# Kernel optimization log

Measured on AMD Instinct MI355X. Metric: run time of the kernel, lower is better.

Reference implementation:

```python
import jax, jax.numpy as jnp
import numpy as np

N, E, H, IN_NF, G, STEPS, EHID = 4096, 8192, 128, 64, 8, 3, 32


def setup_inputs() -> dict:
    key = jax.random.key(0)
    ks = jax.random.split(key, 24)

    def gn(k, shape, fan_in):
        return jax.random.normal(k, shape, dtype=jnp.float32) / np.sqrt(fan_in)

    inp = {
        "x": jax.random.normal(ks[0], (N, IN_NF), dtype=jnp.float32),
        "edge_index": jax.random.randint(ks[1], (2, E), 0, N, dtype=jnp.int32),
        "edge_attr": jax.random.uniform(ks[2], (E, 1), dtype=jnp.float32),
        "batch": jnp.sort(jax.random.randint(ks[3], (N,), 0, G, dtype=jnp.int32)),
        # lin0: in_nf -> hid
        "lin0_w": gn(ks[4], (IN_NF, H), IN_NF),
        "lin0_b": jnp.zeros((H,), jnp.float32),
        # per-step edge MLP: 1 -> 32 -> H*H (stacked over STEPS)
        "nn_w1": gn(ks[5], (STEPS, 1, EHID), 1),
        "nn_b1": jnp.zeros((STEPS, EHID), jnp.float32),
        "nn_w2": gn(ks[6], (STEPS, EHID, H * H), EHID) * 0.1,
        "nn_b2": jnp.zeros((STEPS, H * H), jnp.float32),
        # NNConv root weight (no bias) + conv bias, per step
        "root_w": gn(ks[7], (STEPS, H, H), H),
        "conv_b": jnp.zeros((STEPS, H), jnp.float32),
        # single-layer GRU (input H, hidden H); gate order r, z, n
        "gru_wih": gn(ks[8], (3 * H, H), H),
        "gru_whh": gn(ks[9], (3 * H, H), H),
        "gru_bih": jnp.zeros((3 * H,), jnp.float32),
        "gru_bhh": jnp.zeros((3 * H,), jnp.float32),
        # readout
        "lin1_w": gn(ks[10], (H, H // 2), H),
        "lin1_b": jnp.zeros((H // 2,), jnp.float32),
        "lin2_w": gn(ks[11], (H // 2, 1), H // 2),
        "lin2_b": jnp.zeros((1,), jnp.float32),
    }
    return inp


def _gru_cell(m, h, wih, whh, bih, bhh):
    gi = m @ wih.T + bih          # [N, 3H]
    gh = h @ whh.T + bhh          # [N, 3H]
    i_r, i_z, i_n = jnp.split(gi, 3, axis=-1)
    h_r, h_z, h_n = jnp.split(gh, 3, axis=-1)
    r = jax.nn.sigmoid(i_r + h_r)
    z = jax.nn.sigmoid(i_z + h_z)
    n = jnp.tanh(i_n + r * h_n)
    return (1.0 - z) * n + z * h


def reference(x, edge_index, edge_attr, batch, lin0_w, lin0_b, nn_w1, nn_b1,
              nn_w2, nn_b2, root_w, conv_b, gru_wih, gru_whh, gru_bih,
              gru_bhh, lin1_w, lin1_b, lin2_w, lin2_b):
    n_nodes = x.shape[0]
    row, col = edge_index[0], edge_index[1]  # source j -> target i

    x = jax.nn.relu(x @ lin0_w + lin0_b)     # [N, H]
    h = x

    # in-degree for mean aggregation (0-degree nodes -> 0 output)
    deg = jax.ops.segment_sum(jnp.ones((row.shape[0],), x.dtype), col,
                              num_segments=n_nodes)
    inv_deg = jnp.where(deg > 0, 1.0 / jnp.maximum(deg, 1.0), 0.0)[:, None]

    for t in range(STEPS):
        # edge-conditioned weights: [E, H, H]
        e_h = jax.nn.relu(edge_attr @ nn_w1[t] + nn_b1[t])
        w_e = (e_h @ nn_w2[t] + nn_b2[t]).reshape(-1, H, H)
        # gather -> per-edge matvec -> scatter-mean
        msg = jnp.einsum('eh,eho->eo', x[row], w_e)
        agg = jax.ops.segment_sum(msg, col, num_segments=n_nodes) * inv_deg
        m = jax.nn.relu(agg + x @ root_w[t] + conv_b[t])
        h = _gru_cell(m, h, gru_wih, gru_whh, gru_bih, gru_bhh)
        x = h

    # global mean pool over graphs
    cnt = jax.ops.segment_sum(jnp.ones((n_nodes,), x.dtype), batch,
                              num_segments=G)
    g = jax.ops.segment_sum(x, batch, num_segments=G) / jnp.maximum(cnt, 1.0)[:, None]
    g = jax.nn.relu(g @ lin1_w + lin1_b)  # dropout: eval mode (identity)
    out = g @ lin2_w + lin2_b             # [G, 1]
    return out
```

## Files before the change

kernel.cpp:

```cpp
#include <hip/hip_runtime.h>
#include <math.h>

#define NN 4096
#define EE 8192
#define HH 128
#define GG 8
#define ULD 4352

typedef __attribute__((ext_vector_type(8))) _Float16 half8;
typedef __attribute__((ext_vector_type(4))) float floatx4;

__device__ __forceinline__ void ldst16(const _Float16* g, void* l) {
    __builtin_amdgcn_global_load_lds(
        (const __attribute__((address_space(1))) unsigned int*)g,
        (__attribute__((address_space(3))) unsigned int*)l, 16, 0, 0);
}

__global__ __launch_bounds__(256) void mgemm16_k(
    const _Float16* __restrict__ A, const _Float16* __restrict__ B,
    _Float16* __restrict__ C, const int* __restrict__ kflag)
{
    const int kk = blockIdx.x;
    int cbase;
    if (kk < 32) {
        const unsigned f = *(const unsigned*)kflag;
        if (!((f >> kk) & 1u)) return;
        cbase = __popc(f & ((1u << kk) - 1u)) << 7;
    } else {
        cbase = kk << 7;
    }

    __shared__ __align__(16) _Float16 As[128 * 32];
    __shared__ __align__(16) _Float16 Bs[128 * 32];
    const int tid = threadIdx.x;
    const int lane = tid & 63, wave = tid >> 6;
    const int m0 = blockIdx.y * 128, n0 = kk * 128;
    const int wr = (wave >> 1) * 64, wc = (wave & 1) * 64;
    const int fm = lane & 15, fq = lane >> 4;

    const int srow = tid >> 2, soff = (tid & 3) << 3;
    const _Float16* gA0 = A + (size_t)(m0 + srow) * 128 + soff;
    const _Float16* gA1 = gA0 + (size_t)64 * 128;
    const _Float16* gB0 = B + (size_t)(n0 + srow) * 128 + soff;
    const _Float16* gB1 = gB0 + (size_t)64 * 128;
    char* lA0 = (char*)As + tid * 16;  char* lA1 = (char*)As + (tid + 256) * 16;
    char* lB0 = (char*)Bs + tid * 16;  char* lB1 = (char*)Bs + (tid + 256) * 16;

    floatx4 acc[4][4] = {};
    for (int k0 = 0; k0 < 128; k0 += 32) {
        __syncthreads();
        ldst16(gA0 + k0, lA0); ldst16(gA1 + k0, lA1);
        ldst16(gB0 + k0, lB0); ldst16(gB1 + k0, lB1);
        __syncthreads();
        half8 af[4], bf[4];
#pragma unroll
        for (int i = 0; i < 4; ++i)
            af[i] = *(const half8*)&As[(wr + i * 16 + fm) * 32 + fq * 8];
#pragma unroll
        for (int j = 0; j < 4; ++j)
            bf[j] = *(const half8*)&Bs[(wc + j * 16 + fm) * 32 + fq * 8];
#pragma unroll
        for (int i = 0; i < 4; ++i)
#pragma unroll
            for (int j = 0; j < 4; ++j)
                acc[i][j] = __builtin_amdgcn_mfma_f32_16x16x32_f16(
                    af[i], bf[j], acc[i][j], 0, 0, 0);
    }
    const int er = fq * 4, ec = fm;
#pragma unroll
    for (int i = 0; i < 4; ++i) {
        const int gr = m0 + wr + i * 16 + er;
#pragma unroll
        for (int j = 0; j < 4; ++j) {
            const int gc = cbase + wc + j * 16 + ec;
#pragma unroll
            for (int r = 0; r < 4; ++r)
                C[(size_t)(gr + r) * ULD + gc] = (_Float16)acc[i][j][r];
        }
    }
}

__global__ __launch_bounds__(256) void gru_k(
    const _Float16* __restrict__ bigC, const float* __restrict__ agg,
    const float* __restrict__ cb, const _Float16* __restrict__ Ax,
    const _Float16* __restrict__ Bih, const _Float16* __restrict__ Bhh,
    const float* __restrict__ bih, const float* __restrict__ bhh,
    float* __restrict__ g1, float* __restrict__ g2)
{
    const int z = blockIdx.z;
    const _Float16* B = z ? Bhh : Bih;
    const float* bias = z ? bhh : bih;
    float* C = z ? g2 : g1;

    __shared__ __align__(16) _Float16 As[128 * 40];
    __shared__ __align__(16) _Float16 Bs[128 * 40];
    const int tid = threadIdx.x;
    const int lane = tid & 63, wave = tid >> 6;
    const int m0 = blockIdx.y * 128, n0 = blockIdx.x * 128;
    const int wr = (wave >> 1) * 64, wc = (wave & 1) * 64;
    const int fm = lane & 15, fq = lane >> 4;

    floatx4 acc[4][4] = {};
    for (int k0 = 0; k0 < 128; k0 += 32) {
        __syncthreads();
#pragma unroll
        for (int c = tid; c < 512; c += 256) {
            const int row = c >> 2, seg = (c & 3) << 3;
            if (z == 0) {
                const int mr = m0 + row;
                const half8 cv = *(const half8*)&bigC[(size_t)mr * ULD + 4224 + k0 + seg];
                const float4 a0 = *(const float4*)&agg[(size_t)mr * 128 + k0 + seg];
                const float4 a1 = *(const float4*)&agg[(size_t)mr * 128 + k0 + seg + 4];
                const float4 c0 = *(const float4*)&cb[k0 + seg];
                const float4 c1 = *(const float4*)&cb[k0 + seg + 4];
                _Float16 v8[8];
                float v;
                v = (float)cv[0] + a0.x + c0.x; v8[0] = (_Float16)(v > 0.f ? v : 0.f);
                v = (float)cv[1] + a0.y + c0.y; v8[1] = (_Float16)(v > 0.f ? v : 0.f);
                v = (float)cv[2] + a0.z + c0.z; v8[2] = (_Float16)(v > 0.f ? v : 0.f);
                v = (float)cv[3] + a0.w + c0.w; v8[3] = (_Float16)(v > 0.f ? v : 0.f);
                v = (float)cv[4] + a1.x + c1.x; v8[4] = (_Float16)(v > 0.f ? v : 0.f);
                v = (float)cv[5] + a1.y + c1.y; v8[5] = (_Float16)(v > 0.f ? v : 0.f);
                v = (float)cv[6] + a1.z + c1.z; v8[6] = (_Float16)(v > 0.f ? v : 0.f);
                v = (float)cv[7] + a1.w + c1.w; v8[7] = (_Float16)(v > 0.f ? v : 0.f);
                *(half8*)&As[row * 40 + seg] = *(half8*)v8;
            } else {
                *(half8*)&As[row * 40 + seg] =
                    *(const half8*)&Ax[(size_t)(m0 + row) * 128 + k0 + seg];
            }
            *(half8*)&Bs[row * 40 + seg] =
                *(const half8*)&B[(size_t)(n0 + row) * 128 + k0 + seg];
        }
        __syncthreads();
        half8 af[4], bf[4];
#pragma unroll
        for (int i = 0; i < 4; ++i)
            af[i] = *(const half8*)&As[(wr + i * 16 + fm) * 40 + fq * 8];
#pragma unroll
        for (int j = 0; j < 4; ++j)
            bf[j] = *(const half8*)&Bs[(wc + j * 16 + fm) * 40 + fq * 8];
#pragma unroll
        for (int i = 0; i < 4; ++i)
#pragma unroll
            for (int j = 0; j < 4; ++j)
                acc[i][j] = __builtin_amdgcn_mfma_f32_16x16x32_f16(
                    af[i], bf[j], acc[i][j], 0, 0, 0);
    }
    const int er = fq * 4, ec = fm;
#pragma unroll
    for (int i = 0; i < 4; ++i) {
        const int gr = m0 + wr + i * 16 + er;
#pragma unroll
        for (int j = 0; j < 4; ++j) {
            const int gc = n0 + wc + j * 16 + ec;
            const float bv = bias[gc];
#pragma unroll
            for (int r = 0; r < 4; ++r)
                C[(size_t)(gr + r) * 384 + gc] = acc[i][j][r] + bv;
        }
    }
}

__global__ void gate_k(const float* __restrict__ G1, const float* __restrict__ G2,
                       float* __restrict__ xh, _Float16* __restrict__ Ax,
                       const int* __restrict__ batch, float* __restrict__ pooled) {
    const int idx = blockIdx.x * 256 + threadIdx.x;
    const int n = idx >> 7, o = idx & 127;
    const size_t b = (size_t)n * 384;
    float ir = G1[b + o], iz = G1[b + 128 + o], in_ = G1[b + 256 + o];
    float hr = G2[b + o], hz = G2[b + 128 + o], hn = G2[b + 256 + o];
    float r = 1.f / (1.f + expf(-(ir + hr)));
    float z = 1.f / (1.f + expf(-(iz + hz)));
    float nv = tanhf(in_ + r * hn);
    float hv = (1.f - z) * nv + z * xh[idx];
    xh[idx] = hv;
    Ax[idx] = (_Float16)hv;
    if (pooled) atomicAdd(&pooled[batch[n] * 128 + o], hv);
}

__global__ __launch_bounds__(256) void setup_lin0_k(
    const float* __restrict__ wih, const float* __restrict__ whh,
    _Float16* __restrict__ Bih, _Float16* __restrict__ Bhh,
    const int* __restrict__ ei, const int* __restrict__ batch,
    float* __restrict__ deg, int* __restrict__ odeg, float* __restrict__ cnt,
    const float* __restrict__ x, const float* __restrict__ l0w,
    const float* __restrict__ l0b, float* __restrict__ xh,
    _Float16* __restrict__ Ax)
{
    __shared__ float loc8[GG];
    __shared__ float As[16][64];
    __shared__ float Bs[16][64];
    const int b = blockIdx.x, t = threadIdx.x;
    if (b < 192) {
        const int idx = b * 256 + t;
        Bih[idx] = (_Float16)wih[idx];
        Bhh[idx] = (_Float16)whh[idx];
    } else if (b < 224) {
        const int e = (b - 192) * 256 + t;
        atomicAdd(&deg[ei[EE + e]], 1.0f);
        atomicAdd(&odeg[ei[e]], 1);
    } else if (b < 240) {
        const int n = (b - 224) * 256 + t;
        if (t < GG) loc8[t] = 0.f;
        __syncthreads();
        atomicAdd(&loc8[batch[n]], 1.0f);
        __syncthreads();
        if (t < GG) atomicAdd(&cnt[t], loc8[t]);
    } else {
        const int bb = b - 240;
        const int j0 = (bb & 1) * 64;
        const int m0 = (bb >> 1) * 64;
        const int tx = t & 15, ty = t >> 4;
        const int arow = t >> 2, acol = (t & 3) << 2;
        const int bk = t >> 4, bj = (t & 15) << 2;
        float c[4][4] = {};
        for (int k0 = 0; k0 < 64; k0 += 16) {
            __syncthreads();
            float4 av = *(const float4*)&x[(size_t)(m0 + arow) * 64 + k0 + acol];
            As[acol + 0][arow] = av.x;
            As[acol + 1][arow] = av.y;
            As[acol + 2][arow] = av.z;
            As[acol + 3][arow] = av.w;
            *(float4*)&Bs[bk][bj] = *(const float4*)&l0w[(size_t)(k0 + bk) * 128 + j0 + bj];
            __syncthreads();
#pragma unroll
            for (int kk = 0; kk < 16; ++kk) {
                const float4 a = *(const float4*)&As[kk][ty << 2];
                const float4 bv = *(const float4*)&Bs[kk][tx << 2];
                c[0][0] += a.x * bv.x; c[0][1] += a.x * bv.y; c[0][2] += a.x * bv.z; c[0][3] += a.x * bv.w;
                c[1][0] += a.y * bv.x; c[1][1] += a.y * bv.y; c[1][2] += a.y * bv.z; c[1][3] += a.y * bv.w;
                c[2][0] += a.z * bv.x; c[2][1] += a.z * bv.y; c[2][2] += a.z * bv.z; c[2][3] += a.z * bv.w;
                c[3][0] += a.w * bv.x; c[3][1] += a.w * bv.y; c[3][2] += a.w * bv.z; c[3][3] += a.w * bv.w;
            }
        }
        const float4 bv = *(const float4*)&l0b[j0 + (tx << 2)];
        const int col0 = j0 + (tx << 2);
#pragma unroll
        for (int i = 0; i < 4; ++i) {
            const int row = m0 + (ty << 2) + i;
            float4 o;
            o.x = fmaxf(c[i][0] + bv.x, 0.f); o.y = fmaxf(c[i][1] + bv.y, 0.f);
            o.z = fmaxf(c[i][2] + bv.z, 0.f); o.w = fmaxf(c[i][3] + bv.w, 0.f);
            *(float4*)&xh[(size_t)row * 128 + col0] = o;
            _Float16* base = Ax + (size_t)row * 128 + col0;
            base[0] = (_Float16)o.x; base[1] = (_Float16)o.y;
            base[2] = (_Float16)o.z; base[3] = (_Float16)o.w;
        }
    }
}

__global__ __launch_bounds__(256) void scan_convb_k(
    const int* __restrict__ odeg, int* __restrict__ ocur,
    const float* __restrict__ w2, const float* __restrict__ b2,
    const float* __restrict__ rw, _Float16* __restrict__ BT)
{
    __shared__ int ps[256];
    const int t = threadIdx.x;
    if (blockIdx.x == 0) {
        const int base = t * 16;
        int l[16]; int s = 0;
#pragma unroll
        for (int i = 0; i < 16; ++i) { l[i] = s; s += odeg[base + i]; }
        ps[t] = s;
        __syncthreads();
        for (int d = 1; d < 256; d <<= 1) {
            int v = (t >= d) ? ps[t - d] : 0;
            __syncthreads();
            ps[t] += v;
            __syncthreads();
        }
        const int excl = (t == 0) ? 0 : ps[t - 1];
#pragma unroll
        for (int i = 0; i < 16; ++i) ocur[base + i] = excl + l[i];
    } else {
        const int bb = blockIdx.x - 1;
        const int tt = bb / 2176;
        const int idx = (bb % 2176) * 256 + t;
        const int j = idx >> 7, h = idx & 127;
        float v;
        if (j < 4096)      v = w2[(size_t)tt * 524288 + (size_t)(j >> 7) * 16384 + h * 128 + (j & 127)];
        else if (j < 4224) v = b2[tt * 16384 + h * 128 + (j - 4096)];
        else               v = rw[tt * 16384 + h * 128 + (j - 4224)];
        BT[(size_t)tt * 557056 + (size_t)j * 128 + h] = (_Float16)v;
    }
}

__global__ __launch_bounds__(256) void scatter_k(
    const int* __restrict__ ei, const float* __restrict__ eattr,
    const float* __restrict__ w1, const float* __restrict__ b1,
    const float* __restrict__ deg, int* __restrict__ ocur,
    int2* __restrict__ rc, float* __restrict__ ehP, int* __restrict__ kflag)
{
    __shared__ unsigned bm[3];
    if (threadIdx.x < 3) bm[threadIdx.x] = 0u;
    __syncthreads();
    const int wave = threadIdx.x >> 6, lane = threadIdx.x & 63;
    const int e = blockIdx.x * 4 + wave;
    const int r = ei[e], c = ei[EE + e];
    int pos = 0;
    if (lane == 0) pos = atomicAdd(&ocur[r], 1);
    pos = __shfl(pos, 0);
    if (lane == 0) rc[pos] = make_int2(r, c);
    const float d = deg[c];
    const float inv = d > 0.f ? 1.0f / d : 0.0f;
    const float ea = eattr[e];
#pragma unroll
    for (int t = 0; t < 3; ++t) {
        float w = inv;
        if (lane < 32) {
            float v = ea * w1[t * 32 + lane] + b1[t * 32 + lane];
            w = (v > 0.f ? v : 0.f) * inv;
        }
        const unsigned long long mb = __ballot(lane < 32 && w != 0.f);
        if (lane < 33) ehP[((size_t)t * EE + pos) * 33 + lane] = w;
        if (lane == 0 && (unsigned)mb) atomicOr(&bm[t], (unsigned)mb);
    }
    __syncthreads();
    if (threadIdx.x < 3 && bm[threadIdx.x])
        atomicOr((unsigned*)&kflag[threadIdx.x], bm[threadIdx.x]);
}

__global__ __launch_bounds__(256) void edge_msg_k(
    const int2* __restrict__ rc, const float* __restrict__ ehP,
    const _Float16* __restrict__ U, float* __restrict__ agg,
    const int* __restrict__ kflag)
{
    __shared__ float eh[2][33];
    __shared__ unsigned char kls[32];
    const int b = blockIdx.x;
    const int p0 = ((b & 7) * 512 + (b >> 3)) * 2;
    const int half = threadIdx.x >> 7;
    const int o = threadIdx.x & 127;
    const unsigned f = *(const unsigned*)kflag;
    if (threadIdx.x < 32 && ((f >> threadIdx.x) & 1u))
        kls[__popc(f & ((1u << threadIdx.x) - 1u))] = (unsigned char)threadIdx.x;
    if (o < 33) eh[half][o] = ehP[(size_t)(p0 + half) * 33 + o];
    __syncthreads();
    const int nk = __popc(f);
    const int2 e = rc[p0 + half];
    const _Float16* Ur = U + (size_t)e.x * ULD;
    float acc = eh[half][32] * (float)Ur[4096 + o];
#pragma unroll 4
    for (int i = 0; i < nk; ++i)
        acc += eh[half][kls[i]] * (float)Ur[i * 128 + o];
    atomicAdd(&agg[(size_t)e.y * 128 + o], acc);
}

__global__ __launch_bounds__(128) void final_k(
    const float* __restrict__ pooled, const float* __restrict__ cnt,
    const float* __restrict__ l1w, const float* __restrict__ l1b,
    const float* __restrict__ l2w, const float* __restrict__ l2b,
    float* __restrict__ out)
{
    __shared__ float gv[128];
    const int g = blockIdx.x, t = threadIdx.x;
    float c = cnt[g]; c = c > 1.f ? c : 1.f;
    gv[t] = pooled[g * 128 + t] / c;
    __syncthreads();
    if (t < 64) {
        float y = l1b[t];
        for (int h = 0; h < 128; ++h) y += gv[h] * l1w[h * 64 + t];
        y = y > 0.f ? y : 0.f;
        float s = y * l2w[t];
#pragma unroll
        for (int off = 32; off > 0; off >>= 1)
            s += __shfl_down(s, off);
        if (t == 0) out[g] = s + l2b[0];
    }
}

extern "C" void kernel_launch(void* const* d_in, const int* in_sizes, int n_in,
                              void* d_out, int out_size, void* d_ws, size_t ws_size,
                              hipStream_t stream) {
    const float* x      = (const float*)d_in[0];
    const int*   ei     = (const int*)d_in[1];
    const float* eattr  = (const float*)d_in[2];
    const int*   batch  = (const int*)d_in[3];
    const float* lin0_w = (const float*)d_in[4];
    const float* lin0_b = (const float*)d_in[5];
    const float* nn_w1  = (const float*)d_in[6];
    const float* nn_b1  = (const float*)d_in[7];
    const float* nn_w2  = (const float*)d_in[8];
    const float* nn_b2  = (const float*)d_in[9];
    const float* root_w = (const float*)d_in[10];
    const float* conv_b = (const float*)d_in[11];
    const float* gwih   = (const float*)d_in[12];
    const float* gwhh   = (const float*)d_in[13];
    const float* gbih   = (const float*)d_in[14];
    const float* gbhh   = (const float*)d_in[15];
    const float* l1w    = (const float*)d_in[16];
    const float* l1b    = (const float*)d_in[17];
    const float* l2w    = (const float*)d_in[18];
    const float* l2b    = (const float*)d_in[19];
    float* out = (float*)d_out;
    float* ws  = (float*)d_ws;

    float*    agg0   = ws;
    float*    pooled = ws + 1572864;
    float*    cnt    = ws + 1573888;
    float*    deg    = ws + 1573896;
    int*      odeg   = (int*)(ws + 1577992);
    int*      kflag  = (int*)(ws + 1582088);
    int*      ocur   = (int*)(ws + 1582096);
    int2*     rc     = (int2*)(ws + 1586192);
    float*    ehP    = ws + 1602576;
    float*    xh     = ws + 2413584;
    float*    g1     = ws + 2937872;
    float*    g2     = ws + 4510736;
    _Float16* bigC   = (_Float16*)(ws + 6083600);
    _Float16* Ax     = (_Float16*)(ws + 14996496);
    _Float16* BTu    = (_Float16*)(ws + 15258640);
    _Float16* Bih16  = (_Float16*)(ws + 16094224);
    _Float16* Bhh16  = (_Float16*)(ws + 16118800);

    hipMemsetAsync(agg0, 0, 6328384, stream);
    setup_lin0_k<<<368, 256, 0, stream>>>(gwih, gwhh, Bih16, Bhh16, ei, batch,
                                          deg, odeg, cnt, x, lin0_w, lin0_b,
                                          xh, Ax);
    scan_convb_k<<<6529, 256, 0, stream>>>(odeg, ocur, nn_w2, nn_b2, root_w, BTu);
    scatter_k<<<2048, 256, 0, stream>>>(ei, eattr, nn_w1, nn_b1, deg, ocur, rc, ehP, kflag);

    for (int t = 0; t < 3; ++t) {
        float* agg = agg0 + (size_t)t * 524288;
        mgemm16_k<<<dim3(34, 32), 256, 0, stream>>>(Ax, BTu + (size_t)t * 557056, bigC, kflag + t);
        edge_msg_k<<<EE / 2, 256, 0, stream>>>(rc, ehP + (size_t)t * EE * 33, bigC, agg, kflag + t);
        gru_k<<<dim3(3, 32, 2), 256, 0, stream>>>(bigC, agg, conv_b + t * 128, Ax,
                                                  Bih16, Bhh16, gbih, gbhh, g1, g2);
        gate_k<<<2048, 256, 0, stream>>>(g1, g2, xh, Ax, batch,
                                         (t == 2) ? pooled : nullptr);
    }

    final_k<<<GG, 128, 0, stream>>>(pooled, cnt, l1w, l1b, l2w, l2b, out);
}
```

Before: 265.0 us.

## Split edge MLP units by sign range to collapse always-active units into dense GEMM

Uses the global min/max of edge_attr to classify each hidden ReLU unit of the edge MLP as always-off, always-linear, or mixed. Linear units are folded algebraically into two summed weight matrices applied to per-node aggregates P and Q (scatter of eh*x). Only mixed units still need the per-edge U gather, and the root GEMM plus the GRU input GEMM are fused into one kernel. This removes most of the large per-node U GEMM and the per-edge gathers, at the cost of extra atomics into PQ and a serial block that carries more work in the GRU kernel.

New measurement: 267.0 us. About the same (+0.8%).

```diff
diff --git a/kernel.cpp b/kernel.cpp
--- a/kernel.cpp
+++ b/kernel.cpp
@@ -5,7 +5,7 @@
 #define EE 8192
 #define HH 128
 #define GG 8
-#define ULD 4352
+#define MU 4096
 
 typedef __attribute__((ext_vector_type(8))) _Float16 half8;
 typedef __attribute__((ext_vector_type(4))) float floatx4;
@@ -16,41 +16,58 @@
         (__attribute__((address_space(3))) unsigned int*)l, 16, 0, 0);
 }
 
-__global__ __launch_bounds__(256) void mgemm16_k(
-    const _Float16* __restrict__ A, const _Float16* __restrict__ B,
+__device__ __forceinline__ unsigned f2u(float f) {
+    unsigned b = __float_as_uint(f);
+    return (b & 0x80000000u) ? ~b : (b | 0x80000000u);
+}
+__device__ __forceinline__ float u2f(unsigned u) {
+    return __uint_as_float((u & 0x80000000u) ? (u ^ 0x80000000u) : ~u);
+}
+
+__device__ __forceinline__ int cls_k(float w, float b, float mn, float mx) {
+    const float hi = w > 0.f ? w * mx + b : w * mn + b;
+    const float lo = w > 0.f ? w * mn + b : w * mx + b;
+    if (hi <= 0.f) return 0;
+    if (lo >= 0.f) return 1;
+    return 2;
+}
+
+__global__ __launch_bounds__(256) void mgemm_mixed_k(
+    const _Float16* __restrict__ A, const float* __restrict__ w2,
     _Float16* __restrict__ C, const int* __restrict__ kflag)
 {
+    const unsigned f = *(const unsigned*)kflag;
     const int kk = blockIdx.x;
-    int cbase;
-    if (kk < 32) {
-        const unsigned f = *(const unsigned*)kflag;
-        if (!((f >> kk) & 1u)) return;
-        cbase = __popc(f & ((1u << kk) - 1u)) << 7;
-    } else {
-        cbase = kk << 7;
-    }
+    if (!((f >> kk) & 1u)) return;
+    const int cbase = __popc(f & ((1u << kk) - 1u)) << 7;
 
     __shared__ __align__(16) _Float16 As[128 * 32];
     __shared__ __align__(16) _Float16 Bs[128 * 32];
     const int tid = threadIdx.x;
     const int lane = tid & 63, wave = tid >> 6;
-    const int m0 = blockIdx.y * 128, n0 = kk * 128;
+    const int m0 = blockIdx.y * 128;
     const int wr = (wave >> 1) * 64, wc = (wave & 1) * 64;
     const int fm = lane & 15, fq = lane >> 4;
 
     const int srow = tid >> 2, soff = (tid & 3) << 3;
     const _Float16* gA0 = A + (size_t)(m0 + srow) * 128 + soff;
     const _Float16* gA1 = gA0 + (size_t)64 * 128;
-    const _Float16* gB0 = B + (size_t)(n0 + srow) * 128 + soff;
-    const _Float16* gB1 = gB0 + (size_t)64 * 128;
     char* lA0 = (char*)As + tid * 16;  char* lA1 = (char*)As + (tid + 256) * 16;
-    char* lB0 = (char*)Bs + tid * 16;  char* lB1 = (char*)Bs + (tid + 256) * 16;
+    const float* w2s = w2 + (size_t)kk * 16384;
 
     floatx4 acc[4][4] = {};
     for (int k0 = 0; k0 < 128; k0 += 32) {
         __syncthreads();
         ldst16(gA0 + k0, lA0); ldst16(gA1 + k0, lA1);
-        ldst16(gB0 + k0, lB0); ldst16(gB1 + k0, lB1);
+#pragma unroll
+        for (int c = tid; c < 512; c += 256) {
+            const int row = c >> 2, seg = (c & 3) << 3;
+            _Float16 v8[8];
+#pragma unroll
+            for (int u = 0; u < 8; ++u)
+                v8[u] = (_Float16)w2s[(size_t)(k0 + seg + u) * 128 + row];
+            *(half8*)&Bs[row * 32 + seg] = *(half8*)v8;
+        }
         __syncthreads();
         half8 af[4], bf[4];
 #pragma unroll
@@ -75,88 +92,192 @@
             const int gc = cbase + wc + j * 16 + ec;
 #pragma unroll
             for (int r = 0; r < 4; ++r)
-                C[(size_t)(gr + r) * ULD + gc] = (_Float16)acc[i][j][r];
-        }
-    }
-}
-
-__global__ __launch_bounds__(256) void gru_k(
-    const _Float16* __restrict__ bigC, const float* __restrict__ agg,
-    const float* __restrict__ cb, const _Float16* __restrict__ Ax,
+                C[(size_t)(gr + r) * MU + gc] = (_Float16)acc[i][j][r];
+        }
+    }
+}
+
+__global__ __launch_bounds__(256) void pq_k(
+    const int2* __restrict__ rc, const float* __restrict__ ehP,
+    const float* __restrict__ xh, const _Float16* __restrict__ U,
+    float* __restrict__ PQ, float* __restrict__ agg,
+    const int* __restrict__ kflag)
+{
+    __shared__ float eh[2][34];
+    __shared__ unsigned char kls[32];
+    const int b = blockIdx.x;
+    const int p0 = ((b & 7) * 512 + (b >> 3)) * 2;
+    const int half = threadIdx.x >> 7;
+    const int o = threadIdx.x & 127;
+    const unsigned f = *(const unsigned*)kflag;
+    if (f && threadIdx.x < 32 && ((f >> threadIdx.x) & 1u))
+        kls[__popc(f & ((1u << threadIdx.x) - 1u))] = (unsigned char)threadIdx.x;
+    if (o < 34) eh[half][o] = ehP[(size_t)(p0 + half) * 34 + o];
+    __syncthreads();
+    const int2 e = rc[p0 + half];
+    const float xv = xh[(size_t)e.x * 128 + o];
+    atomicAdd(&PQ[(size_t)e.y * 256 + o], eh[half][33] * xv);
+    atomicAdd(&PQ[(size_t)e.y * 256 + 128 + o], eh[half][32] * xv);
+    if (f) {
+        const int nk = __popc(f);
+        const _Float16* Ur = U + (size_t)e.x * MU;
+        float acc = 0.f;
+        for (int i = 0; i < nk; ++i)
+            acc += eh[half][kls[i]] * (float)Ur[i * 128 + o];
+        atomicAdd(&agg[(size_t)e.y * 128 + o], acc);
+    }
+}
+
+__global__ __launch_bounds__(256) void gru2_k(
+    const float* __restrict__ PQ, const _Float16* __restrict__ BT2t,
+    const float* __restrict__ cb, const float* __restrict__ agg,
+    const _Float16* __restrict__ Ax,
     const _Float16* __restrict__ Bih, const _Float16* __restrict__ Bhh,
     const float* __restrict__ bih, const float* __restrict__ bhh,
-    float* __restrict__ g1, float* __restrict__ g2)
-{
-    const int z = blockIdx.z;
-    const _Float16* B = z ? Bhh : Bih;
-    const float* bias = z ? bhh : bih;
-    float* C = z ? g2 : g1;
-
+    float* __restrict__ g1, float* __restrict__ g2,
+    const int* __restrict__ kflag)
+{
     __shared__ __align__(16) _Float16 As[128 * 40];
     __shared__ __align__(16) _Float16 Bs[128 * 40];
+    __shared__ __align__(16) _Float16 Ms[128 * 136];
     const int tid = threadIdx.x;
     const int lane = tid & 63, wave = tid >> 6;
-    const int m0 = blockIdx.y * 128, n0 = blockIdx.x * 128;
+    const int m0 = blockIdx.y * 128;
     const int wr = (wave >> 1) * 64, wc = (wave & 1) * 64;
     const int fm = lane & 15, fq = lane >> 4;
-
-    floatx4 acc[4][4] = {};
-    for (int k0 = 0; k0 < 128; k0 += 32) {
-        __syncthreads();
-#pragma unroll
-        for (int c = tid; c < 512; c += 256) {
-            const int row = c >> 2, seg = (c & 3) << 3;
-            if (z == 0) {
-                const int mr = m0 + row;
-                const half8 cv = *(const half8*)&bigC[(size_t)mr * ULD + 4224 + k0 + seg];
-                const float4 a0 = *(const float4*)&agg[(size_t)mr * 128 + k0 + seg];
-                const float4 a1 = *(const float4*)&agg[(size_t)mr * 128 + k0 + seg + 4];
-                const float4 c0 = *(const float4*)&cb[k0 + seg];
-                const float4 c1 = *(const float4*)&cb[k0 + seg + 4];
-                _Float16 v8[8];
-                float v;
-                v = (float)cv[0] + a0.x + c0.x; v8[0] = (_Float16)(v > 0.f ? v : 0.f);
-                v = (float)cv[1] + a0.y + c0.y; v8[1] = (_Float16)(v > 0.f ? v : 0.f);
-                v = (float)cv[2] + a0.z + c0.z; v8[2] = (_Float16)(v > 0.f ? v : 0.f);
-                v = (float)cv[3] + a0.w + c0.w; v8[3] = (_Float16)(v > 0.f ? v : 0.f);
-                v = (float)cv[4] + a1.x + c1.x; v8[4] = (_Float16)(v > 0.f ? v : 0.f);
-                v = (float)cv[5] + a1.y + c1.y; v8[5] = (_Float16)(v > 0.f ? v : 0.f);
-                v = (float)cv[6] + a1.z + c1.z; v8[6] = (_Float16)(v > 0.f ? v : 0.f);
-                v = (float)cv[7] + a1.w + c1.w; v8[7] = (_Float16)(v > 0.f ? v : 0.f);
-                *(half8*)&As[row * 40 + seg] = *(half8*)v8;
-            } else {
+    const int er = fq * 4, ec = fm;
+
+    if (blockIdx.x == 0) {
+        floatx4 acc[4][4] = {};
+        for (int k0 = 0; k0 < 384; k0 += 32) {
+            __syncthreads();
+#pragma unroll
+            for (int c = tid; c < 512; c += 256) {
+                const int row = c >> 2, seg = (c & 3) << 3;
+                if (k0 < 256) {
+                    const float4 a0 = *(const float4*)&PQ[(size_t)(m0 + row) * 256 + k0 + seg];
+                    const float4 a1 = *(const float4*)&PQ[(size_t)(m0 + row) * 256 + k0 + seg + 4];
+                    _Float16 v8[8];
+                    v8[0] = (_Float16)a0.x; v8[1] = (_Float16)a0.y;
+                    v8[2] = (_Float16)a0.z; v8[3] = (_Float16)a0.w;
+                    v8[4] = (_Float16)a1.x; v8[5] = (_Float16)a1.y;
+                    v8[6] = (_Float16)a1.z; v8[7] = (_Float16)a1.w;
+                    *(half8*)&As[row * 40 + seg] = *(half8*)v8;
+                } else {
+                    *(half8*)&As[row * 40 + seg] =
+                        *(const half8*)&Ax[(size_t)(m0 + row) * 128 + (k0 - 256) + seg];
+                }
+                *(half8*)&Bs[row * 40 + seg] =
+                    *(const half8*)&BT2t[(size_t)row * 384 + k0 + seg];
+            }
+            __syncthreads();
+            half8 af[4], bf[4];
+#pragma unroll
+            for (int i = 0; i < 4; ++i)
+                af[i] = *(const half8*)&As[(wr + i * 16 + fm) * 40 + fq * 8];
+#pragma unroll
+            for (int j = 0; j < 4; ++j)
+                bf[j] = *(const half8*)&Bs[(wc + j * 16 + fm) * 40 + fq * 8];
+#pragma unroll
+            for (int i = 0; i < 4; ++i)
+#pragma unroll
+                for (int j = 0; j < 4; ++j)
+                    acc[i][j] = __builtin_amdgcn_mfma_f32_16x16x32_f16(
+                        af[i], bf[j], acc[i][j], 0, 0, 0);
+        }
+        const unsigned f = *(const unsigned*)kflag;
+#pragma unroll
+        for (int i = 0; i < 4; ++i) {
+            const int lr = wr + i * 16 + er;
+#pragma unroll
+            for (int j = 0; j < 4; ++j) {
+                const int gc = wc + j * 16 + ec;
+                const float cbv = cb[gc];
+#pragma unroll
+                for (int r = 0; r < 4; ++r) {
+                    float v = acc[i][j][r] + cbv;
+                    if (f) v += agg[(size_t)(m0 + lr + r) * 128 + gc];
+                    Ms[(lr + r) * 136 + gc] = (_Float16)(v > 0.f ? v : 0.f);
+                }
+            }
+        }
+        for (int n0 = 0; n0 < 384; n0 += 128) {
+            floatx4 a2[4][4] = {};
+            for (int k0 = 0; k0 < 128; k0 += 32) {
+                __syncthreads();
+#pragma unroll
+                for (int c = tid; c < 512; c += 256) {
+                    const int row = c >> 2, seg = (c & 3) << 3;
+                    *(half8*)&Bs[row * 40 + seg] =
+                        *(const half8*)&Bih[(size_t)(n0 + row) * 128 + k0 + seg];
+                }
+                __syncthreads();
+                half8 af[4], bf[4];
+#pragma unroll
+                for (int i = 0; i < 4; ++i)
+                    af[i] = *(const half8*)&Ms[(wr + i * 16 + fm) * 136 + k0 + fq * 8];
+#pragma unroll
+                for (int j = 0; j < 4; ++j)
+                    bf[j] = *(const half8*)&Bs[(wc + j * 16 + fm) * 40 + fq * 8];
+#pragma unroll
+                for (int i = 0; i < 4; ++i)
+#pragma unroll
+                    for (int j = 0; j < 4; ++j)
+                        a2[i][j] = __builtin_amdgcn_mfma_f32_16x16x32_f16(
+                            af[i], bf[j], a2[i][j], 0, 0, 0);
+            }
+#pragma unroll
+            for (int i = 0; i < 4; ++i) {
+                const int gr = m0 + wr + i * 16 + er;
+#pragma unroll
+                for (int j = 0; j < 4; ++j) {
+                    const int gc = wc + j * 16 + ec;
+                    const float bv = bih[n0 + gc];
+#pragma unroll
+                    for (int r = 0; r < 4; ++r)
+                        g1[(size_t)(gr + r) * 384 + n0 + gc] = a2[i][j][r] + bv;
+                }
+            }
+        }
+    } else {
+        const int n0 = (blockIdx.x - 1) * 128;
+        floatx4 acc[4][4] = {};
+        for (int k0 = 0; k0 < 128; k0 += 32) {
+            __syncthreads();
+#pragma unroll
+            for (int c = tid; c < 512; c += 256) {
+                const int row = c >> 2, seg = (c & 3) << 3;
                 *(half8*)&As[row * 40 + seg] =
                     *(const half8*)&Ax[(size_t)(m0 + row) * 128 + k0 + seg];
-            }
-            *(half8*)&Bs[row * 40 + seg] =
-                *(const half8*)&B[(size_t)(n0 + row) * 128 + k0 + seg];
-        }
-        __syncthreads();
-        half8 af[4], bf[4];
-#pragma unroll
-        for (int i = 0; i < 4; ++i)
-            af[i] = *(const half8*)&As[(wr + i * 16 + fm) * 40 + fq * 8];
-#pragma unroll
-        for (int j = 0; j < 4; ++j)
-            bf[j] = *(const half8*)&Bs[(wc + j * 16 + fm) * 40 + fq * 8];
-#pragma unroll
-        for (int i = 0; i < 4; ++i)
+                *(half8*)&Bs[row * 40 + seg] =
+                    *(const half8*)&Bhh[(size_t)(n0 + row) * 128 + k0 + seg];
+            }
+            __syncthreads();
+            half8 af[4], bf[4];
+#pragma unroll
+            for (int i = 0; i < 4; ++i)
+                af[i] = *(const half8*)&As[(wr + i * 16 + fm) * 40 + fq * 8];
 #pragma unroll
             for (int j = 0; j < 4; ++j)
-                acc[i][j] = __builtin_amdgcn_mfma_f32_16x16x32_f16(
-                    af[i], bf[j], acc[i][j], 0, 0, 0);
-    }
-    const int er = fq * 4, ec = fm;
-#pragma unroll
-    for (int i = 0; i < 4; ++i) {
-        const int gr = m0 + wr + i * 16 + er;
-#pragma unroll
-        for (int j = 0; j < 4; ++j) {
-            const int gc = n0 + wc + j * 16 + ec;
-            const float bv = bias[gc];
-#pragma unroll
-            for (int r = 0; r < 4; ++r)
-                C[(size_t)(gr + r) * 384 + gc] = acc[i][j][r] + bv;
+                bf[j] = *(const half8*)&Bs[(wc + j * 16 + fm) * 40 + fq * 8];
+#pragma unroll
+            for (int i = 0; i < 4; ++i)
+#pragma unroll
+                for (int j = 0; j < 4; ++j)
+                    acc[i][j] = __builtin_amdgcn_mfma_f32_16x16x32_f16(
+                        af[i], bf[j], acc[i][j], 0, 0, 0);
+        }
+#pragma unroll
+        for (int i = 0; i < 4; ++i) {
+            const int gr = m0 + wr + i * 16 + er;
+#pragma unroll
+            for (int j = 0; j < 4; ++j) {
+                const int gc = wc + j * 16 + ec;
+                const float bv = bhh[n0 + gc];
+#pragma unroll
+                for (int r = 0; r < 4; ++r)
+                    g2[(size_t)(gr + r) * 384 + n0 + gc] = acc[i][j][r] + bv;
+            }
         }
     }
 }
@@ -181,8 +302,10 @@
 __global__ __launch_bounds__(256) void setup_lin0_k(
     const float* __restrict__ wih, const float* __restrict__ whh,
     _Float16* __restrict__ Bih, _Float16* __restrict__ Bhh,
-    const int* __restrict__ ei, const int* __restrict__ batch,
+    const int* __restrict__ ei, const float* __restrict__ eattr,
+    const int* __restrict__ batch,
     float* __restrict__ deg, int* __restrict__ odeg, float* __restrict__ cnt,
+    unsigned* __restrict__ eaMM,
     const float* __restrict__ x, const float* __restrict__ l0w,
     const float* __restrict__ l0b, float* __restrict__ xh,
     _Float16* __restrict__ Ax)
@@ -199,6 +322,14 @@
         const int e = (b - 192) * 256 + t;
         atomicAdd(&deg[ei[EE + e]], 1.0f);
         atomicAdd(&odeg[ei[e]], 1);
+        const float ea = eattr[e];
+        unsigned u1 = f2u(ea), u2 = f2u(-ea);
+#pragma unroll
+        for (int off = 32; off > 0; off >>= 1) {
+            unsigned o1 = __shfl_down(u1, off), o2 = __shfl_down(u2, off);
+            u1 = u1 > o1 ? u1 : o1;  u2 = u2 > o2 ? u2 : o2;
+        }
+        if ((t & 63) == 0) { atomicMax(&eaMM[0], u1); atomicMax(&eaMM[1], u2); }
     } else if (b < 240) {
         const int n = (b - 224) * 256 + t;
         if (t < GG) loc8[t] = 0.f;
@@ -249,14 +380,16 @@
     }
 }
 
-__global__ __launch_bounds__(256) void scan_convb_k(
+__global__ __launch_bounds__(256) void scan_wsum_k(
     const int* __restrict__ odeg, int* __restrict__ ocur,
+    const float* __restrict__ w1, const float* __restrict__ b1,
     const float* __restrict__ w2, const float* __restrict__ b2,
-    const float* __restrict__ rw, _Float16* __restrict__ BT)
-{
-    __shared__ int ps[256];
+    const float* __restrict__ rw, const unsigned* __restrict__ eaMM,
+    _Float16* __restrict__ BT2)
+{
     const int t = threadIdx.x;
     if (blockIdx.x == 0) {
+        __shared__ int ps[256];
         const int base = t * 16;
         int l[16]; int s = 0;
 #pragma unroll
@@ -273,15 +406,31 @@
 #pragma unroll
         for (int i = 0; i < 16; ++i) ocur[base + i] = excl + l[i];
     } else {
+        __shared__ float wl[32], bl[32];
         const int bb = blockIdx.x - 1;
-        const int tt = bb / 2176;
-        const int idx = (bb % 2176) * 256 + t;
-        const int j = idx >> 7, h = idx & 127;
-        float v;
-        if (j < 4096)      v = w2[(size_t)tt * 524288 + (size_t)(j >> 7) * 16384 + h * 128 + (j & 127)];
-        else if (j < 4224) v = b2[tt * 16384 + h * 128 + (j - 4096)];
-        else               v = rw[tt * 16384 + h * 128 + (j - 4224)];
-        BT[(size_t)tt * 557056 + (size_t)j * 128 + h] = (_Float16)v;
+        const int st = bb >> 6;
+        if (t < 32) {
+            const float w = w1[st * 32 + t], bv = b1[st * 32 + t];
+            const float mx = u2f(eaMM[0]), mn = -u2f(eaMM[1]);
+            const int c = cls_k(w, bv, mn, mx);
+            wl[t] = (c == 1) ? w : 0.f;
+            bl[t] = (c == 1) ? bv : 0.f;
+        }
+        __syncthreads();
+        const int idx = (bb & 63) * 256 + t;
+        const int h = idx >> 7, o = idx & 127;
+        const float* W2t = w2 + (size_t)st * 524288;
+        float a = 0.f, c2 = 0.f;
+#pragma unroll 8
+        for (int j = 0; j < 32; ++j) {
+            const float v = W2t[(size_t)j * 16384 + idx];
+            a += wl[j] * v; c2 += bl[j] * v;
+        }
+        c2 += b2[(size_t)st * 16384 + idx];
+        _Float16* B = BT2 + (size_t)st * 49152 + (size_t)o * 384;
+        B[h]       = (_Float16)a;
+        B[128 + h] = (_Float16)c2;
+        B[256 + h] = (_Float16)rw[(size_t)st * 16384 + idx];
     }
 }
 
@@ -289,11 +438,18 @@
     const int* __restrict__ ei, const float* __restrict__ eattr,
     const float* __restrict__ w1, const float* __restrict__ b1,
     const float* __restrict__ deg, int* __restrict__ ocur,
+    const unsigned* __restrict__ eaMM,
     int2* __restrict__ rc, float* __restrict__ ehP, int* __restrict__ kflag)
 {
-    __shared__ unsigned bm[3];
-    if (threadIdx.x < 3) bm[threadIdx.x] = 0u;
+    __shared__ unsigned mm[3];
+    if (threadIdx.x < 3) mm[threadIdx.x] = 0u;
     __syncthreads();
+    if (threadIdx.x < 96) {
+        const int tt = threadIdx.x >> 5, k = threadIdx.x & 31;
+        const float w = w1[tt * 32 + k], bv = b1[tt * 32 + k];
+        const float mx = u2f(eaMM[0]), mn = -u2f(eaMM[1]);
+        if (cls_k(w, bv, mn, mx) == 2) atomicOr(&mm[tt], 1u << k);
+    }
     const int wave = threadIdx.x >> 6, lane = threadIdx.x & 63;
     const int e = blockIdx.x * 4 + wave;
     const int r = ei[e], c = ei[EE + e];
@@ -306,44 +462,17 @@
     const float ea = eattr[e];
 #pragma unroll
     for (int t = 0; t < 3; ++t) {
-        float w = inv;
+        float w;
         if (lane < 32) {
-            float v = ea * w1[t * 32 + lane] + b1[t * 32 + lane];
+            const float v = ea * w1[t * 32 + lane] + b1[t * 32 + lane];
             w = (v > 0.f ? v : 0.f) * inv;
-        }
-        const unsigned long long mb = __ballot(lane < 32 && w != 0.f);
-        if (lane < 33) ehP[((size_t)t * EE + pos) * 33 + lane] = w;
-        if (lane == 0 && (unsigned)mb) atomicOr(&bm[t], (unsigned)mb);
+        } else {
+            w = (lane == 32) ? inv : ea * inv;
+        }
+        if (lane < 34) ehP[((size_t)t * EE + pos) * 34 + lane] = w;
     }
     __syncthreads();
-    if (threadIdx.x < 3 && bm[threadIdx.x])
-        atomicOr((unsigned*)&kflag[threadIdx.x], bm[threadIdx.x]);
-}
-
-__global__ __launch_bounds__(256) void edge_msg_k(
-    const int2* __restrict__ rc, const float* __restrict__ ehP,
-    const _Float16* __restrict__ U, float* __restrict__ agg,
-    const int* __restrict__ kflag)
-{
-    __shared__ float eh[2][33];
-    __shared__ unsigned char kls[32];
-    const int b = blockIdx.x;
-    const int p0 = ((b & 7) * 512 + (b >> 3)) * 2;
-    const int half = threadIdx.x >> 7;
-    const int o = threadIdx.x & 127;
-    const unsigned f = *(const unsigned*)kflag;
-    if (threadIdx.x < 32 && ((f >> threadIdx.x) & 1u))
-        kls[__popc(f & ((1u << threadIdx.x) - 1u))] = (unsigned char)threadIdx.x;
-    if (o < 33) eh[half][o] = ehP[(size_t)(p0 + half) * 33 + o];
-    __syncthreads();
-    const int nk = __popc(f);
-    const int2 e = rc[p0 + half];
-    const _Float16* Ur = U + (size_t)e.x * ULD;
-    float acc = eh[half][32] * (float)Ur[4096 + o];
-#pragma unroll 4
-    for (int i = 0; i < nk; ++i)
-        acc += eh[half][kls[i]] * (float)Ur[i * 128 + o];
-    atomicAdd(&agg[(size_t)e.y * 128 + o], acc);
+    if (threadIdx.x < 3) kflag[threadIdx.x] = (int)mm[threadIdx.x];
 }
 
 __global__ __launch_bounds__(128) void final_k(
@@ -396,36 +525,45 @@
     float* ws  = (float*)d_ws;
 
     float*    agg0   = ws;
-    float*    pooled = ws + 1572864;
-    float*    cnt    = ws + 1573888;
-    float*    deg    = ws + 1573896;
-    int*      odeg   = (int*)(ws + 1577992);
-    int*      kflag  = (int*)(ws + 1582088);
-    int*      ocur   = (int*)(ws + 1582096);
-    int2*     rc     = (int2*)(ws + 1586192);
-    float*    ehP    = ws + 1602576;
-    float*    xh     = ws + 2413584;
-    float*    g1     = ws + 2937872;
-    float*    g2     = ws + 4510736;
-    _Float16* bigC   = (_Float16*)(ws + 6083600);
-    _Float16* Ax     = (_Float16*)(ws + 14996496);
-    _Float16* BTu    = (_Float16*)(ws + 15258640);
-    _Float16* Bih16  = (_Float16*)(ws + 16094224);
-    _Float16* Bhh16  = (_Float16*)(ws + 16118800);
-
-    hipMemsetAsync(agg0, 0, 6328384, stream);
-    setup_lin0_k<<<368, 256, 0, stream>>>(gwih, gwhh, Bih16, Bhh16, ei, batch,
-                                          deg, odeg, cnt, x, lin0_w, lin0_b,
-                                          xh, Ax);
-    scan_convb_k<<<6529, 256, 0, stream>>>(odeg, ocur, nn_w2, nn_b2, root_w, BTu);
-    scatter_k<<<2048, 256, 0, stream>>>(ei, eattr, nn_w1, nn_b1, deg, ocur, rc, ehP, kflag);
+    float*    PQ0    = ws + 1572864;
+    float*    pooled = ws + 4718592;
+    float*    cnt    = ws + 4719616;
+    float*    deg    = ws + 4719624;
+    int*      odeg   = (int*)(ws + 4723720);
+    unsigned* eaMM   = (unsigned*)(ws + 4727816);
+    int*      kflag  = (int*)(ws + 4727818);
+    int*      ocur   = (int*)(ws + 4727824);
+    int2*     rc     = (int2*)(ws + 4731920);
+    float*    ehP    = ws + 4748304;
+    float*    xh     = ws + 5583888;
+    _Float16* bigC   = (_Float16*)(ws + 6108176);
+    _Float16* Ax     = (_Float16*)(ws + 14496784);
+    _Float16* BT2    = (_Float16*)(ws + 14758928);
+    _Float16* Bih16  = (_Float16*)(ws + 14832656);
+    _Float16* Bhh16  = (_Float16*)(ws + 14857232);
+    float*    g1     = ws + 14881808;
+    float*    g2     = ws + 16454672;
+
+    hipMemsetAsync(agg0, 0, 18911296, stream);
+    setup_lin0_k<<<368, 256, 0, stream>>>(gwih, gwhh, Bih16, Bhh16, ei, eattr,
+                                          batch, deg, odeg, cnt, eaMM,
+                                          x, lin0_w, lin0_b, xh, Ax);
+    scan_wsum_k<<<193, 256, 0, stream>>>(odeg, ocur, nn_w1, nn_b1, nn_w2,
+                                         nn_b2, root_w, eaMM, BT2);
+    scatter_k<<<2048, 256, 0, stream>>>(ei, eattr, nn_w1, nn_b1, deg, ocur,
+                                        eaMM, rc, ehP, kflag);
 
     for (int t = 0; t < 3; ++t) {
         float* agg = agg0 + (size_t)t * 524288;
-        mgemm16_k<<<dim3(34, 32), 256, 0, stream>>>(Ax, BTu + (size_t)t * 557056, bigC, kflag + t);
-        edge_msg_k<<<EE / 2, 256, 0, stream>>>(rc, ehP + (size_t)t * EE * 33, bigC, agg, kflag + t);
-        gru_k<<<dim3(3, 32, 2), 256, 0, stream>>>(bigC, agg, conv_b + t * 128, Ax,
-                                                  Bih16, Bhh16, gbih, gbhh, g1, g2);
+        float* PQ  = PQ0 + (size_t)t * 1048576;
+        mgemm_mixed_k<<<dim3(32, 32), 256, 0, stream>>>(
+            Ax, nn_w2 + (size_t)t * 524288, bigC, kflag + t);
+        pq_k<<<EE / 2, 256, 0, stream>>>(rc, ehP + (size_t)t * EE * 34, xh,
+                                         bigC, PQ, agg, kflag + t);
+        gru2_k<<<dim3(4, 32), 256, 0, stream>>>(PQ, BT2 + (size_t)t * 49152,
+                                                conv_b + t * 128, agg, Ax,
+                                                Bih16, Bhh16, gbih, gbhh,
+                                                g1, g2, kflag + t);
         gate_k<<<2048, 256, 0, stream>>>(g1, g2, xh, Ax, batch,
                                          (t == 2) ? pooled : nullptr);
     }
```
